# Performance work log

Measured on AMD Instinct MI355X. Metric: run time of the kernel, lower is better.

## Reference

```python
import jax, jax.numpy as jnp
import numpy as np

N, D_IN, D_H, D_A, K = 131072, 768, 128, 32, 64
BN_EPS = 1e-5

def setup_inputs() -> dict:
    key = jax.random.key(0)
    ks = jax.random.split(key, 16)
    def lin(k, fan_in, shape):
        return (jax.random.uniform(k, shape, jnp.float32, -1.0, 1.0) / np.sqrt(fan_in)).astype(jnp.float32)
    return {
        "input": jax.random.normal(ks[0], (1, N, D_IN), jnp.float32),
        # linear: Linear(768,128) + BN(128)
        "W1": lin(ks[1], D_IN, (D_IN, D_H)), "b1": lin(ks[2], D_IN, (D_H,)),
        "g1": jnp.ones((D_H,), jnp.float32), "be1": jnp.zeros((D_H,), jnp.float32),
        # attention: Linear(128,32) + BN(32) + Tanh + Linear(32,1)
        "Watt1": lin(ks[3], D_H, (D_H, D_A)), "batt1": lin(ks[4], D_H, (D_A,)),
        "g2": jnp.ones((D_A,), jnp.float32), "be2": jnp.zeros((D_A,), jnp.float32),
        "Watt2": lin(ks[5], D_A, (D_A, 1)), "batt2": lin(ks[6], D_A, (1,)),
        # Wa ModuleList: three Linear(128,32, bias=False)
        "Wq": lin(ks[7], D_H, (D_H, D_A)),
        "Wk": lin(ks[8], D_H, (D_H, D_A)),
        "Wv": lin(ks[9], D_H, (D_H, D_A)),
        # linear_z: Linear(32*k, 128)
        "Wz": lin(ks[10], D_A * K, (D_A * K, D_H)), "bz": lin(ks[11], D_A * K, (D_H,)),
        # fc: Linear(128, 1)
        "Wf": lin(ks[12], D_H, (D_H, 1)), "bf": lin(ks[13], D_H, (1,)),
    }

def reference(input, W1, b1, g1, be1, Watt1, batt1, g2, be2, Watt2, batt2,
              Wq, Wk, Wv, Wz, bz, Wf, bf):
    k = Wz.shape[0] // D_A  # static
    inv = 1.0 / jnp.sqrt(1.0 + BN_EPS)  # BN eval: running_mean=0, running_var=1
    x = input[0]  # [N, 768]
    x = jax.nn.relu((x @ W1 + b1) * (g1 * inv) + be1)  # [N, 128]
    h = jnp.tanh((x @ Watt1 + batt1) * (g2 * inv) + be2)  # [N, 32]
    A = jax.nn.softmax((h @ Watt2 + batt2)[:, 0], axis=0)  # [N]
    order = jnp.argsort(-A)           # descending sort indices
    A_sorted = A[order]
    zs = x[order[:k]] * jax.nn.softmax(A_sorted[:k])[:, None]  # [k, 128]
    zq, zk_, zv = zs @ Wq, zs @ Wk, zs @ Wv                    # [k, 32] each
    zw = jax.nn.softmax(zq @ zk_.T, axis=1) @ zv               # [k, 32]
    zw = jax.nn.relu(zw.reshape(1, -1) @ Wz + bz)              # [1, 128]
    return zw @ Wf + bf                                        # [1, 1]
```

## Files before the change

### kernel.cpp

```cpp
#include <hip/hip_runtime.h>


#define NN   131072
#define DIN  768
#define DH   128
#define DA   32

using f32x4  = __attribute__((ext_vector_type(4))) float;
using bf16x8 = __attribute__((ext_vector_type(8))) __bf16;

#define WS_S      0
#define WS_PZ8    524288
#define WS_HIST   557056
#define WS_MISC   573440
#define WS_CIDX   573504
#define WS_CS     575552
#define WS_ORDER  577600
#define WS_W      577856
#define WS_ZQ     578112
#define WS_ZK     586304
#define WS_ZV     594496
#define WS_ZW     602688
#define WS_W1T    610944

__device__ __forceinline__ int s_bin(float s) {
  int b = (int)((s + 6.0f) * (4096.0f / 12.0f));
  return b < 0 ? 0 : (b > 4095 ? 4095 : b);
}

__device__ __forceinline__ void gl_lds16(const void* g, void* l) {
  __builtin_amdgcn_global_load_lds(
      (const __attribute__((address_space(1))) void*)g,
      (__attribute__((address_space(3))) void*)l, 16, 0, 0);
}

__global__ void k_prep(const float* __restrict__ W1, char* __restrict__ ws) {
  int T = blockIdx.x * 256 + threadIdx.x;
  if (T < 4112) ((int*)(ws + WS_HIST))[T] = 0;
  int u = T & 7, col = (T >> 3) & 127, kc = T >> 10;
  bf16x8 ov;
  #pragma unroll
  for (int j = 0; j < 8; ++j) {
    int k = (u & 3) * 8 + j;
    float v = W1[(size_t)(kc * 32 + k) * 128 + col];
    __bf16 h = (__bf16)v;
    ov[j] = (u < 4) ? h : (__bf16)(v - (float)h);
  }
  *(bf16x8*)(ws + WS_W1T + (size_t)kc * 16384 + col * 128 + u * 16) = ov;
}

__global__ __launch_bounds__(256, 3) void k_main(
    const float* __restrict__ inp,
    const float* __restrict__ b1, const float* __restrict__ g1, const float* __restrict__ be1,
    const float* __restrict__ Watt1, const float* __restrict__ batt1,
    const float* __restrict__ g2, const float* __restrict__ be2,
    const float* __restrict__ Watt2, const float* __restrict__ batt2,
    char* __restrict__ ws)
{
  __shared__ __align__(16) char lds[49152];
  float* s_out = (float*)(ws + WS_S);
  float* pz8   = (float*)(ws + WS_PZ8);
  int*   hist  = (int*)(ws + WS_HIST);
  const char* w1t = ws + WS_W1T;

  const int t = threadIdx.x;
  const int l = t & 63;
  const int wid = t >> 6;
  const int wr = wid >> 1, wc = wid & 1;
  const int blockRow = blockIdx.x * 128;
  const float inv = 1.0f / sqrtf(1.0f + 1e-5f);

  char* Ab0 = lds;
  char* Ab1 = lds + 16384;
  char* xh  = lds;
  float* wat = (float*)(lds + 32768);

  const int sr = t >> 3;
  const int su = (t & 7) ^ (sr & 7);
  const float* aSrc = inp + (size_t)(blockRow + sr) * DIN + su * 4;
  #pragma unroll
  for (int c = 0; c < 4; ++c)
    gl_lds16(Watt1 + c * 1024 + t * 4, (char*)wat + c * 4096 + t * 16);
  #pragma unroll
  for (int c = 0; c < 4; ++c)
    gl_lds16(aSrc + (size_t)c * 24576, Ab0 + c * 4096 + t * 16);

  f32x4 acc[4][4];
  #pragma unroll
  for (int i = 0; i < 4; ++i)
    #pragma unroll
    for (int j = 0; j < 4; ++j)
      #pragma unroll
      for (int q = 0; q < 4; ++q) acc[i][j][q] = 0.0f;

  const int kg = l >> 4, r15 = l & 15;
  for (int kc = 0; kc < 24; ++kc) {
    const char* A = (kc & 1) ? Ab1 : Ab0;
    char* An = (kc & 1) ? Ab0 : Ab1;
    asm volatile("s_waitcnt vmcnt(0)" ::: "memory");
    __builtin_amdgcn_sched_barrier(0);
    __builtin_amdgcn_s_barrier();
    __builtin_amdgcn_sched_barrier(0);

    bf16x8 ahi[4], alo[4];
    #pragma unroll
    for (int mi = 0; mi < 4; ++mi) {
      int R = wr * 64 + mi * 16 + r15;
      const char* base = A + R * 128; int sw = R & 7;
      f32x4 a0 = *(const f32x4*)(base + (((kg * 2)     ^ sw) << 4));
      f32x4 a1 = *(const f32x4*)(base + (((kg * 2 + 1) ^ sw) << 4));
      #pragma unroll
      for (int j = 0; j < 4; ++j) {
        float x0 = a0[j]; __bf16 h0 = (__bf16)x0;
        ahi[mi][j] = h0;     alo[mi][j] = (__bf16)(x0 - (float)h0);
        float x1 = a1[j]; __bf16 h1 = (__bf16)x1;
        ahi[mi][4+j] = h1;   alo[mi][4+j] = (__bf16)(x1 - (float)h1);
      }
    }
    __builtin_amdgcn_sched_barrier(0);
    bf16x8 bhi[4], blo[4];
    #pragma unroll
    for (int ni = 0; ni < 4; ++ni) {
      const char* bb = w1t + (size_t)kc * 16384 + (wc * 64 + ni * 16 + r15) * 128;
      bhi[ni] = *(const bf16x8*)(bb + (kg << 4));
      blo[ni] = *(const bf16x8*)(bb + 64 + (kg << 4));
    }
    __builtin_amdgcn_sched_barrier(0);
    if (kc < 23) {
      #pragma unroll
      for (int c = 0; c < 4; ++c)
        gl_lds16(aSrc + (size_t)c * 24576 + (kc + 1) * 32, An + c * 4096 + t * 16);
    }
    __builtin_amdgcn_sched_barrier(0);
    #pragma unroll
    for (int ni = 0; ni < 4; ++ni)
      #pragma unroll
      for (int mi = 0; mi < 4; ++mi) {
        acc[mi][ni] = __builtin_amdgcn_mfma_f32_16x16x32_bf16(ahi[mi], bhi[ni], acc[mi][ni], 0, 0, 0);
        acc[mi][ni] = __builtin_amdgcn_mfma_f32_16x16x32_bf16(ahi[mi], blo[ni], acc[mi][ni], 0, 0, 0);
        acc[mi][ni] = __builtin_amdgcn_mfma_f32_16x16x32_bf16(alo[mi], bhi[ni], acc[mi][ni], 0, 0, 0);
      }
  }

  __syncthreads();
  const int row = t >> 2, q4 = t & 3;
  const int rsw = (row & 31) << 4;
  for (int pass = 0; pass < 2; ++pass) {
    if (wr == pass) {
      #pragma unroll
      for (int ni = 0; ni < 4; ++ni) {
        int col = wc * 64 + ni * 16 + r15;
        float b1c = b1[col], s1c = g1[col] * inv, be1c = be1[col];
        #pragma unroll
        for (int mi = 0; mi < 4; ++mi) {
          #pragma unroll
          for (int q = 0; q < 4; ++q) {
            int rloc = mi * 16 + kg * 4 + q;
            float xv = fmaxf((acc[mi][ni][q] + b1c) * s1c + be1c, 0.0f);
            *(float*)(xh + rloc * 512 + ((col * 4) ^ ((rloc & 31) << 4))) = xv;
          }
        }
      }
    }
    __syncthreads();
    float hacc[8];
    #pragma unroll
    for (int a = 0; a < 8; ++a) hacc[a] = 0.0f;
    const char* xrow = xh + row * 512;
    for (int cb = 0; cb < 128; cb += 4) {
      f32x4 xv = *(const f32x4*)(xrow + ((cb * 4) ^ rsw));
      #pragma unroll
      for (int u = 0; u < 4; ++u) {
        const float* wrow = wat + (cb + u) * 32 + q4 * 8;
        f32x4 w0 = *(const f32x4*)(wrow);
        f32x4 w1 = *(const f32x4*)(wrow + 4);
        float xs = xv[u];
        #pragma unroll
        for (int q = 0; q < 4; ++q) {
          hacc[q]     += xs * w0[q];
          hacc[4 + q] += xs * w1[q];
        }
      }
    }
    float partial = 0.0f;
    #pragma unroll
    for (int a = 0; a < 8; ++a) {
      int ai = q4 * 8 + a;
      float hv = tanhf((hacc[a] + batt1[ai]) * (g2[ai] * inv) + be2[ai]);
      partial += hv * Watt2[ai];
    }
    partial += __shfl_xor(partial, 1, 64);
    partial += __shfl_xor(partial, 2, 64);
    float ev = 0.0f;
    if (q4 == 0) {
      float sv = partial + batt2[0];
      s_out[blockRow + pass * 64 + row] = sv;
      atomicAdd(&hist[s_bin(sv)], 1);
      ev = expf(sv);
    }
    #pragma unroll
    for (int off = 32; off >= 1; off >>= 1) ev += __shfl_xor(ev, off, 64);
    if (l == 0) pz8[blockIdx.x * 8 + pass * 4 + wid] = ev;
    __syncthreads();
  }
}

__global__ void k_reduce(char* __restrict__ ws) {
  float* pz8 = (float*)(ws + WS_PZ8);
  int* hist = (int*)(ws + WS_HIST);
  float* miscf = (float*)(ws + WS_MISC);
  int* misci = (int*)(ws + WS_MISC);
  const int t = threadIdx.x;
  __shared__ float red[256];
  __shared__ int csum[256];
  float z = 0.0f;
  for (int i = t; i < 8192; i += 256) z += pz8[i];
  red[t] = z;
  int c = 0;
  #pragma unroll
  for (int u = 0; u < 16; ++u) c += hist[t * 16 + u];
  csum[t] = c;
  __syncthreads();
  for (int off = 128; off >= 1; off >>= 1) {
    if (t < off) red[t] += red[t + off];
    __syncthreads();
  }
  if (t == 0) {
    miscf[0] = red[0];
    int cum = 0, bstar = 0;
    for (int ch = 255; ch >= 0; --ch) {
      if (cum + csum[ch] >= 64) {
        for (int b = ch * 16 + 15; b >= ch * 16; --b) {
          cum += hist[b];
          if (cum >= 64) { bstar = b; break; }
        }
        break;
      }
      cum += csum[ch];
    }
    misci[3] = bstar;
    misci[2] = 0;
  }
}

__global__ void k_gather(char* __restrict__ ws) {
  const int i = blockIdx.x * 256 + threadIdx.x;
  float* s_out = (float*)(ws + WS_S);
  int* misci = (int*)(ws + WS_MISC);
  int* cidx = (int*)(ws + WS_CIDX);
  float* cs = (float*)(ws + WS_CS);
  float s = s_out[i];
  if (s_bin(s) >= misci[3]) {
    int pos = atomicAdd(&misci[2], 1);
    if (pos < 512) { cidx[pos] = i; cs[pos] = s; }
  }
}

__global__ void k_select(char* __restrict__ ws) {
  const int t = threadIdx.x;
  float* s_out = (float*)(ws + WS_S);
  int* misci = (int*)(ws + WS_MISC);
  float* miscf = (float*)(ws + WS_MISC);
  int* cidx = (int*)(ws + WS_CIDX);
  float* cs = (float*)(ws + WS_CS);
  int* order = (int*)(ws + WS_ORDER);
  float* wsel = (float*)(ws + WS_W);
  __shared__ unsigned long long keys[512];
  __shared__ float aLds[64];
  int cnt = misci[2]; if (cnt > 512) cnt = 512;
  for (int i = t; i < 512; i += 256) {
    unsigned long long kkey = 0xFFFFFFFFFFFFFFFFull;
    if (i < cnt) {
      unsigned u = __float_as_uint(cs[i]);
      u = (u & 0x80000000u) ? ~u : (u | 0x80000000u);
      unsigned du = ~u;
      kkey = ((unsigned long long)du << 32) | (unsigned)cidx[i];
    }
    keys[i] = kkey;
  }
  __syncthreads();
  for (int k = 2; k <= 512; k <<= 1) {
    for (int j = k >> 1; j > 0; j >>= 1) {
      for (int i = t; i < 512; i += 256) {
        int ixj = i ^ j;
        if (ixj > i) {
          bool up = ((i & k) == 0);
          unsigned long long a = keys[i], b2 = keys[ixj];
          if (up ? (a > b2) : (a < b2)) { keys[i] = b2; keys[ixj] = a; }
        }
      }
      __syncthreads();
    }
  }
  float Z = miscf[0];
  if (t < 64) {
    int idx = (int)(keys[t] & 0xFFFFFFFFull);
    order[t] = idx;
    aLds[t] = expf(s_out[idx]) / Z;
  }
  __syncthreads();
  if (t < 64) {
    float m = aLds[0];
    float e = expf(aLds[t] - m);
    float sum = e;
    #pragma unroll
    for (int off = 32; off >= 1; off >>= 1) sum += __shfl_xor(sum, off, 64);
    wsel[t] = e / sum;
  }
}

__global__ void k_zs(const float* __restrict__ inp, const float* __restrict__ W1,
                     const float* __restrict__ b1, const float* __restrict__ g1, const float* __restrict__ be1,
                     const float* __restrict__ Wq, const float* __restrict__ Wk, const float* __restrict__ Wv,
                     char* __restrict__ ws)
{
  const int t = threadIdx.x, b = blockIdx.x;
  int* order = (int*)(ws + WS_ORDER);
  float* wsel = (float*)(ws + WS_W);
  float* zq = (float*)(ws + WS_ZQ);
  float* zk = (float*)(ws + WS_ZK);
  float* zv = (float*)(ws + WS_ZV);
  __shared__ float rowS[768];
  __shared__ float zsS[128];
  const float inv = 1.0f / sqrtf(1.0f + 1e-5f);
  int r = order[b];
  float wgt = wsel[b];
  for (int i = t; i < 768; i += 256) rowS[i] = inp[(size_t)r * 768 + i];
  __syncthreads();
  if (t < 128) {
    float d = 0.0f;
    for (int k = 0; k < 768; ++k) d += rowS[k] * W1[(size_t)k * 128 + t];
    float x = fmaxf((d + b1[t]) * (g1[t] * inv) + be1[t], 0.0f);
    zsS[t] = x * wgt;
  }
  __syncthreads();
  if (t < 96) {
    int which = t >> 5, a = t & 31;
    const float* W = (which == 0) ? Wq : ((which == 1) ? Wk : Wv);
    float d = 0.0f;
    for (int c = 0; c < 128; ++c) d += zsS[c] * W[c * 32 + a];
    float* dst = (which == 0) ? zq : ((which == 1) ? zk : zv);
    dst[b * 32 + a] = d;
  }
}

__global__ void k_attn(char* __restrict__ ws, float* __restrict__ out) {
  const int t = threadIdx.x;
  if (t == 0) out[0] = 0.0f;
  float* zq = (float*)(ws + WS_ZQ);
  float* zk = (float*)(ws + WS_ZK);
  float* zv = (float*)(ws + WS_ZV);
  float* zw = (float*)(ws + WS_ZW);
  __shared__ float q[2048], kk[2048], v[2048], P[4096];
  for (int i = t; i < 2048; i += 256) { q[i] = zq[i]; kk[i] = zk[i]; v[i] = zv[i]; }
  __syncthreads();
  for (int o = t; o < 4096; o += 256) {
    int i = o >> 6, j = o & 63;
    float d = 0.0f;
    for (int a = 0; a < 32; ++a) d += q[i * 32 + a] * kk[j * 32 + a];
    P[o] = d;
  }
  __syncthreads();
  if (t < 64) {
    float m = -1e30f;
    for (int j = 0; j < 64; ++j) m = fmaxf(m, P[t * 64 + j]);
    float sum = 0.0f;
    for (int j = 0; j < 64; ++j) { float e = expf(P[t * 64 + j] - m); P[t * 64 + j] = e; sum += e; }
    float rs = 1.0f / sum;
    for (int j = 0; j < 64; ++j) P[t * 64 + j] *= rs;
  }
  __syncthreads();
  for (int o = t; o < 2048; o += 256) {
    int i = o >> 5, a = o & 31;
    float d = 0.0f;
    for (int j = 0; j < 64; ++j) d += P[i * 64 + j] * v[j * 32 + a];
    zw[o] = d;
  }
}

__global__ void k_wz(const float* __restrict__ Wz, const float* __restrict__ bz,
                     const float* __restrict__ Wf, const float* __restrict__ bf_,
                     char* __restrict__ ws, float* __restrict__ out) {
  const int t = threadIdx.x, j = blockIdx.x;
  float* zw = (float*)(ws + WS_ZW);
  __shared__ float red[256];
  float p = 0.0f;
  for (int i2 = t; i2 < 2048; i2 += 256) p += zw[i2] * Wz[(size_t)i2 * 128 + j];
  red[t] = p; __syncthreads();
  for (int off = 128; off >= 1; off >>= 1) {
    if (t < off) red[t] += red[t + off];
    __syncthreads();
  }
  if (t == 0) {
    float o = fmaxf(red[0] + bz[j], 0.0f);
    float contrib = o * Wf[j] + (j == 0 ? bf_[0] : 0.0f);
    atomicAdd(out, contrib);
  }
}

extern "C" void kernel_launch(void* const* d_in, const int* in_sizes, int n_in,
                              void* d_out, int out_size, void* d_ws, size_t ws_size,
                              hipStream_t stream) {
  const float* inp   = (const float*)d_in[0];
  const float* W1    = (const float*)d_in[1];
  const float* b1    = (const float*)d_in[2];
  const float* g1    = (const float*)d_in[3];
  const float* be1   = (const float*)d_in[4];
  const float* Watt1 = (const float*)d_in[5];
  const float* batt1 = (const float*)d_in[6];
  const float* g2    = (const float*)d_in[7];
  const float* be2   = (const float*)d_in[8];
  const float* Watt2 = (const float*)d_in[9];
  const float* batt2 = (const float*)d_in[10];
  const float* Wq    = (const float*)d_in[11];
  const float* Wk    = (const float*)d_in[12];
  const float* Wv    = (const float*)d_in[13];
  const float* Wz    = (const float*)d_in[14];
  const float* bz    = (const float*)d_in[15];
  const float* Wf    = (const float*)d_in[16];
  const float* bf_   = (const float*)d_in[17];
  char* ws = (char*)d_ws;

  k_prep<<<dim3(96), dim3(256), 0, stream>>>(W1, ws);
  k_main<<<dim3(1024), dim3(256), 0, stream>>>(inp, b1, g1, be1, Watt1, batt1, g2, be2, Watt2, batt2, ws);
  k_reduce<<<dim3(1), dim3(256), 0, stream>>>(ws);
  k_gather<<<dim3(512), dim3(256), 0, stream>>>(ws);
  k_select<<<dim3(1), dim3(256), 0, stream>>>(ws);
  k_zs<<<dim3(64), dim3(256), 0, stream>>>(inp, W1, b1, g1, be1, Wq, Wk, Wv, ws);
  k_attn<<<dim3(1), dim3(256), 0, stream>>>(ws, (float*)d_out);
  k_wz<<<dim3(128), dim3(256), 0, stream>>>(Wz, bz, Wf, bf_, ws, (float*)d_out);
}
```

Before: 352.4 us.

## Restructure main GEMM: stream A from global into registers, stage swizzled W1 in LDS

The main GEMM now uses a 64-row block tile, with each wave owning 16 rows across all 128 columns. Input rows are loaded straight from global memory into registers and prefetched one k-chunk ahead. The pre-split bf16 W1 tiles are DMA'd into double-buffered LDS in a new XOR-swizzled layout to avoid bank conflicts, replacing the old scheme that staged A in LDS and read B from global. The change also halves LDS, raises the occupancy hint to 4, doubles the grid, and reads Watt1 directly from global in the epilogue. The intent is to cut LDS traffic and global B reloads and to improve latency hiding. The cost is more B traffic per row, since W1 is re-fetched for every 64 rows, plus uncoalesced strided A loads.

Result: faster. 324.8 us (-7.8%).

```diff
diff --git a/kernel.cpp b/kernel.cpp
--- a/kernel.cpp
+++ b/kernel.cpp
@@ -46,10 +46,10 @@
     __bf16 h = (__bf16)v;
     ov[j] = (u < 4) ? h : (__bf16)(v - (float)h);
   }
-  *(bf16x8*)(ws + WS_W1T + (size_t)kc * 16384 + col * 128 + u * 16) = ov;
-}
-
-__global__ __launch_bounds__(256, 3) void k_main(
+  *(bf16x8*)(ws + WS_W1T + (size_t)kc * 16384 + col * 128 + ((u ^ (col & 7)) << 4)) = ov;
+}
+
+__global__ __launch_bounds__(256, 4) void k_main(
     const float* __restrict__ inp,
     const float* __restrict__ b1, const float* __restrict__ g1, const float* __restrict__ be1,
     const float* __restrict__ Watt1, const float* __restrict__ batt1,
@@ -57,7 +57,7 @@
     const float* __restrict__ Watt2, const float* __restrict__ batt2,
     char* __restrict__ ws)
 {
-  __shared__ __align__(16) char lds[49152];
+  __shared__ __align__(16) char lds[32768];
   float* s_out = (float*)(ws + WS_S);
   float* pz8   = (float*)(ws + WS_PZ8);
   int*   hist  = (int*)(ws + WS_HIST);
@@ -66,112 +66,101 @@
   const int t = threadIdx.x;
   const int l = t & 63;
   const int wid = t >> 6;
-  const int wr = wid >> 1, wc = wid & 1;
-  const int blockRow = blockIdx.x * 128;
+  const int r15 = l & 15, kg = l >> 4;
+  const int blockRow = blockIdx.x * 64;
   const float inv = 1.0f / sqrtf(1.0f + 1e-5f);
 
-  char* Ab0 = lds;
-  char* Ab1 = lds + 16384;
-  char* xh  = lds;
-  float* wat = (float*)(lds + 32768);
-
-  const int sr = t >> 3;
-  const int su = (t & 7) ^ (sr & 7);
-  const float* aSrc = inp + (size_t)(blockRow + sr) * DIN + su * 4;
+  char* Bb0 = lds;
+  char* Bb1 = lds + 16384;
+
+  const float* aRow = inp + (size_t)(blockRow + wid * 16 + r15) * DIN + kg * 8;
+  const int swzHi = (kg ^ (l & 7)) << 4;
+  const int swzLo = ((4 | kg) ^ (l & 7)) << 4;
+
+  f32x4 acc[8];
   #pragma unroll
-  for (int c = 0; c < 4; ++c)
-    gl_lds16(Watt1 + c * 1024 + t * 4, (char*)wat + c * 4096 + t * 16);
+  for (int i = 0; i < 8; ++i)
+    #pragma unroll
+    for (int q = 0; q < 4; ++q) acc[i][q] = 0.0f;
+
+#define BDMA(Bbuf, kc_) do { \
+    const char* s_ = w1t + (size_t)(kc_) * 16384 + t * 16; \
+    char* d_ = (Bbuf) + t * 16; \
+    gl_lds16(s_, d_); gl_lds16(s_ + 4096, d_ + 4096); \
+    gl_lds16(s_ + 8192, d_ + 8192); gl_lds16(s_ + 12288, d_ + 12288); \
+  } while (0)
+
+#define ITER(Bcur, Bnxt, c0, c1, n0, n1, kc_) do { \
+    if ((kc_) < 23) { \
+      BDMA(Bnxt, (kc_) + 1); \
+      const float* ap_ = aRow + ((kc_) + 1) * 32; \
+      n0 = *(const f32x4*)ap_; n1 = *(const f32x4*)(ap_ + 4); \
+      asm volatile("s_waitcnt vmcnt(6)" ::: "memory"); \
+    } else { \
+      asm volatile("s_waitcnt vmcnt(0)" ::: "memory"); \
+    } \
+    __builtin_amdgcn_sched_barrier(0); \
+    __builtin_amdgcn_s_barrier(); \
+    __builtin_amdgcn_sched_barrier(0); \
+    bf16x8 ahi, alo; \
+    _Pragma("unroll") \
+    for (int j2 = 0; j2 < 4; ++j2) { \
+      float x0 = c0[j2]; __bf16 h0 = (__bf16)x0; \
+      ahi[j2] = h0; alo[j2] = (__bf16)(x0 - (float)h0); \
+      float x1 = c1[j2]; __bf16 h1 = (__bf16)x1; \
+      ahi[4 + j2] = h1; alo[4 + j2] = (__bf16)(x1 - (float)h1); \
+    } \
+    _Pragma("unroll") \
+    for (int ni = 0; ni < 8; ++ni) { \
+      const char* cb_ = (Bcur) + r15 * 128 + ni * 2048; \
+      bf16x8 bhi = *(const bf16x8*)(cb_ + swzHi); \
+      bf16x8 blo = *(const bf16x8*)(cb_ + swzLo); \
+      acc[ni] = __builtin_amdgcn_mfma_f32_16x16x32_bf16(ahi, bhi, acc[ni], 0, 0, 0); \
+      acc[ni] = __builtin_amdgcn_mfma_f32_16x16x32_bf16(ahi, blo, acc[ni], 0, 0, 0); \
+      acc[ni] = __builtin_amdgcn_mfma_f32_16x16x32_bf16(alo, bhi, acc[ni], 0, 0, 0); \
+    } \
+    __builtin_amdgcn_sched_barrier(0); \
+    __builtin_amdgcn_s_barrier(); \
+    __builtin_amdgcn_sched_barrier(0); \
+  } while (0)
+
+  f32x4 pa0, pa1, pb0, pb1;
+  BDMA(Bb0, 0);
+  { const float* ap_ = aRow; pa0 = *(const f32x4*)ap_; pa1 = *(const f32x4*)(ap_ + 4); }
+
+  for (int kc = 0; kc < 24; kc += 2) {
+    ITER(Bb0, Bb1, pa0, pa1, pb0, pb1, kc);
+    ITER(Bb1, Bb0, pb0, pb1, pa0, pa1, kc + 1);
+  }
+#undef ITER
+#undef BDMA
+
   #pragma unroll
-  for (int c = 0; c < 4; ++c)
-    gl_lds16(aSrc + (size_t)c * 24576, Ab0 + c * 4096 + t * 16);
-
-  f32x4 acc[4][4];
-  #pragma unroll
-  for (int i = 0; i < 4; ++i)
-    #pragma unroll
-    for (int j = 0; j < 4; ++j)
-      #pragma unroll
-      for (int q = 0; q < 4; ++q) acc[i][j][q] = 0.0f;
-
-  const int kg = l >> 4, r15 = l & 15;
-  for (int kc = 0; kc < 24; ++kc) {
-    const char* A = (kc & 1) ? Ab1 : Ab0;
-    char* An = (kc & 1) ? Ab0 : Ab1;
-    asm volatile("s_waitcnt vmcnt(0)" ::: "memory");
-    __builtin_amdgcn_sched_barrier(0);
-    __builtin_amdgcn_s_barrier();
-    __builtin_amdgcn_sched_barrier(0);
-
-    bf16x8 ahi[4], alo[4];
-    #pragma unroll
-    for (int mi = 0; mi < 4; ++mi) {
-      int R = wr * 64 + mi * 16 + r15;
-      const char* base = A + R * 128; int sw = R & 7;
-      f32x4 a0 = *(const f32x4*)(base + (((kg * 2)     ^ sw) << 4));
-      f32x4 a1 = *(const f32x4*)(base + (((kg * 2 + 1) ^ sw) << 4));
-      #pragma unroll
-      for (int j = 0; j < 4; ++j) {
-        float x0 = a0[j]; __bf16 h0 = (__bf16)x0;
-        ahi[mi][j] = h0;     alo[mi][j] = (__bf16)(x0 - (float)h0);
-        float x1 = a1[j]; __bf16 h1 = (__bf16)x1;
-        ahi[mi][4+j] = h1;   alo[mi][4+j] = (__bf16)(x1 - (float)h1);
-      }
-    }
-    __builtin_amdgcn_sched_barrier(0);
-    bf16x8 bhi[4], blo[4];
-    #pragma unroll
-    for (int ni = 0; ni < 4; ++ni) {
-      const char* bb = w1t + (size_t)kc * 16384 + (wc * 64 + ni * 16 + r15) * 128;
-      bhi[ni] = *(const bf16x8*)(bb + (kg << 4));
-      blo[ni] = *(const bf16x8*)(bb + 64 + (kg << 4));
-    }
-    __builtin_amdgcn_sched_barrier(0);
-    if (kc < 23) {
-      #pragma unroll
-      for (int c = 0; c < 4; ++c)
-        gl_lds16(aSrc + (size_t)c * 24576 + (kc + 1) * 32, An + c * 4096 + t * 16);
-    }
-    __builtin_amdgcn_sched_barrier(0);
-    #pragma unroll
-    for (int ni = 0; ni < 4; ++ni)
-      #pragma unroll
-      for (int mi = 0; mi < 4; ++mi) {
-        acc[mi][ni] = __builtin_amdgcn_mfma_f32_16x16x32_bf16(ahi[mi], bhi[ni], acc[mi][ni], 0, 0, 0);
-        acc[mi][ni] = __builtin_amdgcn_mfma_f32_16x16x32_bf16(ahi[mi], blo[ni], acc[mi][ni], 0, 0, 0);
-        acc[mi][ni] = __builtin_amdgcn_mfma_f32_16x16x32_bf16(alo[mi], bhi[ni], acc[mi][ni], 0, 0, 0);
-      }
-  }
-
-  __syncthreads();
-  const int row = t >> 2, q4 = t & 3;
-  const int rsw = (row & 31) << 4;
-  for (int pass = 0; pass < 2; ++pass) {
-    if (wr == pass) {
-      #pragma unroll
-      for (int ni = 0; ni < 4; ++ni) {
-        int col = wc * 64 + ni * 16 + r15;
-        float b1c = b1[col], s1c = g1[col] * inv, be1c = be1[col];
-        #pragma unroll
-        for (int mi = 0; mi < 4; ++mi) {
-          #pragma unroll
-          for (int q = 0; q < 4; ++q) {
-            int rloc = mi * 16 + kg * 4 + q;
-            float xv = fmaxf((acc[mi][ni][q] + b1c) * s1c + be1c, 0.0f);
-            *(float*)(xh + rloc * 512 + ((col * 4) ^ ((rloc & 31) << 4))) = xv;
-          }
-        }
-      }
-    }
-    __syncthreads();
+  for (int ni = 0; ni < 8; ++ni) {
+    int col = ni * 16 + r15;
+    float b1c = b1[col], s1c = g1[col] * inv, be1c = be1[col];
+    #pragma unroll
+    for (int q = 0; q < 4; ++q) {
+      int row = wid * 16 + kg * 4 + q;
+      float xv = fmaxf((acc[ni][q] + b1c) * s1c + be1c, 0.0f);
+      *(float*)(lds + row * 512 + ((col * 4) ^ ((row & 31) << 4))) = xv;
+    }
+  }
+  __syncthreads();
+
+  {
+    const int row = t >> 2, q4 = t & 3;
+    const int rsw = (row & 31) << 4;
     float hacc[8];
     #pragma unroll
     for (int a = 0; a < 8; ++a) hacc[a] = 0.0f;
-    const char* xrow = xh + row * 512;
+    const char* xrow = lds + row * 512;
+    const float* watt = Watt1 + q4 * 8;
     for (int cb = 0; cb < 128; cb += 4) {
       f32x4 xv = *(const f32x4*)(xrow + ((cb * 4) ^ rsw));
       #pragma unroll
       for (int u = 0; u < 4; ++u) {
-        const float* wrow = wat + (cb + u) * 32 + q4 * 8;
+        const float* wrow = watt + (cb + u) * 32;
         f32x4 w0 = *(const f32x4*)(wrow);
         f32x4 w1 = *(const f32x4*)(wrow + 4);
         float xs = xv[u];
@@ -194,14 +183,13 @@
     float ev = 0.0f;
     if (q4 == 0) {
       float sv = partial + batt2[0];
-      s_out[blockRow + pass * 64 + row] = sv;
+      s_out[blockRow + row] = sv;
       atomicAdd(&hist[s_bin(sv)], 1);
       ev = expf(sv);
     }
     #pragma unroll
     for (int off = 32; off >= 1; off >>= 1) ev += __shfl_xor(ev, off, 64);
-    if (l == 0) pz8[blockIdx.x * 8 + pass * 4 + wid] = ev;
-    __syncthreads();
+    if (l == 0) pz8[blockIdx.x * 4 + wid] = ev;
   }
 }
 
@@ -422,7 +410,7 @@
   char* ws = (char*)d_ws;
 
   k_prep<<<dim3(96), dim3(256), 0, stream>>>(W1, ws);
-  k_main<<<dim3(1024), dim3(256), 0, stream>>>(inp, b1, g1, be1, Watt1, batt1, g2, be2, Watt2, batt2, ws);
+  k_main<<<dim3(2048), dim3(256), 0, stream>>>(inp, b1, g1, be1, Watt1, batt1, g2, be2, Watt2, batt2, ws);
   k_reduce<<<dim3(1), dim3(256), 0, stream>>>(ws);
   k_gather<<<dim3(512), dim3(256), 0, stream>>>(ws);
   k_select<<<dim3(1), dim3(256), 0, stream>>>(ws);
```
